# Optimization experiments

Measured on AMD Instinct MI355X. Metric: run time of the kernel, lower is better.

Reference implementation:

```python
import jax, jax.numpy as jnp
import numpy as np

N_NODES = 100000
N_EDGES = 1600000
D_IN = 128
D_HID = 128
SCALE = 1.8
EPS = 1e-12


def setup_inputs() -> dict:
    key = jax.random.key(0)
    ks = jax.random.split(key, 7)
    x = jax.random.normal(ks[0], (N_NODES, D_IN), dtype=jnp.float32)
    W1 = jax.random.normal(ks[1], (D_HID, D_IN), dtype=jnp.float32) * 0.05
    b1 = jax.random.normal(ks[2], (D_HID,), dtype=jnp.float32) * 0.05
    W2 = jax.random.normal(ks[3], (D_HID, D_HID), dtype=jnp.float32) * 0.05
    b2 = jax.random.normal(ks[4], (D_HID,), dtype=jnp.float32) * 0.05
    src = jax.random.randint(ks[5], (N_EDGES,), 0, N_NODES, dtype=jnp.int64 if jax.config.jax_enable_x64 else jnp.int32)
    dst = jax.random.randint(ks[6], (N_EDGES,), 0, N_NODES, dtype=jnp.int64 if jax.config.jax_enable_x64 else jnp.int32)
    return {"x": x, "W1": W1, "b1": b1, "W2": W2, "b2": b2, "src": src, "dst": dst}


def reference(x, W1, b1, W2, b2, src, dst):
    N = x.shape[0]
    ones = jnp.ones((src.shape[0],), dtype=x.dtype)
    # GraphConv norm='both' degree normalizers (clamped to >=1 as in DGL)
    deg_out = jnp.maximum(jnp.zeros((N,), x.dtype).at[src].add(ones), 1.0)
    deg_in = jnp.maximum(jnp.zeros((N,), x.dtype).at[dst].add(ones), 1.0)
    norm_out = jax.lax.rsqrt(deg_out)[:, None]  # [N,1]
    norm_in = jax.lax.rsqrt(deg_in)[:, None]    # [N,1]

    def layer(h, W, b):
        # torch.nn.Linear: h @ W.T + b
        h = jnp.einsum('nd,kd->nk', h, W) + b
        # F.normalize(h, dim=1) * 1.8
        nrm = jnp.sqrt(jnp.sum(h * h, axis=1, keepdims=True))
        h = h / jnp.maximum(nrm, EPS) * SCALE
        # GraphConv (weight=False, bias=False, norm='both'):
        # D_out^{-1/2} -> sparse aggregate -> D_in^{-1/2}
        h = h * norm_out
        agg = jax.ops.segment_sum(h[src], dst, num_segments=N)
        return agg * norm_in

    h = layer(x, W1, b1)
    h = layer(h, W2, b2)
    return h
```

## Files before the change

### kernel.cpp

```cpp
#include <hip/hip_runtime.h>
#include <cstdint>
#include <cstddef>

#define D 128
#define NSCALE 1.8f
#define NEPS 1e-12f
#define EPB 4096
#define NLO 512
#define SCAP 9216
#define SSTRIDE 10240
#define SRCB 23
#define SRCM 0x7FFFFF

typedef __attribute__((ext_vector_type(8))) short bf16x8;
typedef __attribute__((ext_vector_type(4))) float f32x4;

__device__ __forceinline__ ushort bf16_rtn(float f) {
    uint32_t u = __float_as_uint(f);
    u = u + 0x7FFFu + ((u >> 16) & 1u);
    return (ushort)(u >> 16);
}

__device__ __forceinline__ float blo(uint32_t u) { return __uint_as_float(u << 16); }
__device__ __forceinline__ float bhi(uint32_t u) { return __uint_as_float(u & 0xFFFF0000u); }

__global__ __launch_bounds__(512) void zero_kernel(int* __restrict__ p) {
    p[threadIdx.x] = 0;
}

__global__ __launch_bounds__(512) void scatter_direct_kernel(const int* __restrict__ src,
                                                             const int* __restrict__ dst,
                                                             int* __restrict__ cnt_d,
                                                             int* __restrict__ cnt_s,
                                                             uint32_t* __restrict__ spack,
                                                             ushort* __restrict__ ss_low,
                                                             int ne) {
    __shared__ int hist[256], sc[256], cur[256], gbase[256];
    __shared__ uint32_t sbuf[EPB];
    __shared__ uint8_t binb[EPB];
    int t = threadIdx.x, b = blockIdx.x;
    int base = b * EPB, end = min(ne, base + EPB), m = end - base;

    int myd[8], mys[8];
    #pragma unroll
    for (int k = 0; k < 8; ++k) {
        int i = base + t + 512 * k;
        bool ok = (i < end);
        myd[k] = ok ? dst[i] : -1;
        mys[k] = ok ? src[i] : -1;
    }

    if (t < 256) hist[t] = 0;
    __syncthreads();
    #pragma unroll
    for (int k = 0; k < 8; ++k)
        if (myd[k] >= 0) atomicAdd(&hist[myd[k] >> 9], 1);
    __syncthreads();
    if (t < 256) sc[t] = hist[t];
    __syncthreads();
    #pragma unroll
    for (int off = 1; off < 256; off <<= 1) {
        int u = (t >= off && t < 256) ? sc[t - off] : 0;
        __syncthreads();
        if (t < 256) sc[t] += u;
        __syncthreads();
    }
    if (t < 256) {
        int c = hist[t];
        int excl = sc[t] - c;
        cur[t] = excl;
        if (c > 0) {
            int ofs = atomicAdd(&cnt_d[t], c);
            gbase[t] = t * SSTRIDE + ofs - excl;
        }
    }
    __syncthreads();
    #pragma unroll
    for (int k = 0; k < 8; ++k) {
        if (myd[k] >= 0) {
            int bin = myd[k] >> 9;
            int pos = atomicAdd(&cur[bin], 1);
            sbuf[pos] = ((uint32_t)(myd[k] & (NLO - 1)) << SRCB) | (uint32_t)mys[k];
            binb[pos] = (uint8_t)bin;
        }
    }
    __syncthreads();
    for (int i = t; i < m; i += 512) {
        int bin = binb[i];
        int gi = gbase[bin] + i;
        if (gi - bin * SSTRIDE < SSTRIDE) spack[gi] = sbuf[i];
    }
    __syncthreads();

    if (t < 256) hist[t] = 0;
    __syncthreads();
    #pragma unroll
    for (int k = 0; k < 8; ++k)
        if (mys[k] >= 0) atomicAdd(&hist[mys[k] >> 9], 1);
    __syncthreads();
    if (t < 256) sc[t] = hist[t];
    __syncthreads();
    #pragma unroll
    for (int off = 1; off < 256; off <<= 1) {
        int u = (t >= off && t < 256) ? sc[t - off] : 0;
        __syncthreads();
        if (t < 256) sc[t] += u;
        __syncthreads();
    }
    if (t < 256) {
        int c = hist[t];
        int excl = sc[t] - c;
        cur[t] = excl;
        if (c > 0) {
            int ofs = atomicAdd(&cnt_s[t], c);
            gbase[t] = t * SSTRIDE + ofs - excl;
        }
    }
    __syncthreads();
    ushort* sb2 = (ushort*)sbuf;
    #pragma unroll
    for (int k = 0; k < 8; ++k) {
        if (mys[k] >= 0) {
            int bin = mys[k] >> 9;
            int pos = atomicAdd(&cur[bin], 1);
            sb2[pos] = (ushort)(mys[k] & (NLO - 1));
            binb[pos] = (uint8_t)bin;
        }
    }
    __syncthreads();
    for (int i = t; i < m; i += 512) {
        int bin = binb[i];
        int gi = gbase[bin] + i;
        if (gi - bin * SSTRIDE < SSTRIDE) ss_low[gi] = sb2[i];
    }
}

__global__ __launch_bounds__(1024) void bucket_sorthist_kernel(const uint32_t* __restrict__ spack,
                                                               const int* __restrict__ cnt_d,
                                                               const ushort* __restrict__ ss_low,
                                                               const int* __restrict__ cnt_s,
                                                               int* __restrict__ offs,
                                                               int* __restrict__ cnt_dst,
                                                               float* __restrict__ norm_in,
                                                               float* __restrict__ norm_out,
                                                               int* __restrict__ ssrc, int N) {
    __shared__ int h[NLO], sc[NLO], cur[NLO];
    __shared__ int inA[SCAP];
    __shared__ int stage[SCAP];
    int t = threadIdx.x, v = blockIdx.x;
    int beg = v * SSTRIDE;

    if (blockIdx.y == 1) {
        int m2 = min(cnt_s[v], SSTRIDE);
        int end = beg + m2;
        if (t < NLO) h[t] = 0;
        __syncthreads();
        for (int i = beg + t; i < end; i += 1024) atomicAdd(&h[(int)ss_low[i]], 1);
        __syncthreads();
        int g = (v << 9) + t;
        if (t < NLO && g < N) norm_out[g] = rsqrtf((float)max(h[t], 1));
        return;
    }

    int m = min(cnt_d[v], SSTRIDE);
    int end = beg + m;
    bool staged = (m <= SCAP);

    if (t < NLO) h[t] = 0;
    if (staged) {
        __syncthreads();
        for (int i = beg + t; i < end; i += 1024) inA[i - beg] = (int)spack[i];
        __syncthreads();
        for (int i = t; i < m; i += 1024) atomicAdd(&h[((uint32_t)inA[i]) >> SRCB], 1);
    } else {
        __syncthreads();
        for (int i = beg + t; i < end; i += 1024) atomicAdd(&h[spack[i] >> SRCB], 1);
    }
    __syncthreads();
    int cnt = 0;
    if (t < NLO) { cnt = h[t]; sc[t] = cnt; }
    __syncthreads();
    #pragma unroll
    for (int off = 1; off < NLO; off <<= 1) {
        int u = (t >= off && t < NLO) ? sc[t - off] : 0;
        __syncthreads();
        if (t < NLO) sc[t] += u;
        __syncthreads();
    }
    int excl = (t < NLO) ? (sc[t] - cnt) : 0;
    int g = (v << 9) + t;
    if (t < NLO && g < N) {
        offs[g] = beg + excl;
        cnt_dst[g] = cnt;
        norm_in[g] = rsqrtf((float)max(cnt, 1));
    }
    if (staged) {
        if (t < NLO) cur[t] = excl;
        __syncthreads();
        for (int i = t; i < m; i += 1024) {
            uint32_t p = (uint32_t)inA[i];
            int pos = atomicAdd(&cur[p >> SRCB], 1);
            stage[pos] = (int)(p & SRCM);
        }
        __syncthreads();
        for (int j = t; j < m; j += 1024) ssrc[beg + j] = stage[j];
    } else {
        if (t < NLO) cur[t] = beg + excl;
        __syncthreads();
        for (int i = beg + t; i < end; i += 1024) {
            uint32_t p = spack[i];
            int pos = atomicAdd(&cur[p >> SRCB], 1);
            ssrc[pos] = (int)(p & SRCM);
        }
    }
}

__global__ __launch_bounds__(256, 2) void mlp_fused_kernel(const float* __restrict__ X,
                                                           const float* __restrict__ W1,
                                                           const float* __restrict__ b1,
                                                           const float* __restrict__ W2,
                                                           const float* __restrict__ post,
                                                           ushort* __restrict__ Q,
                                                           ushort* __restrict__ Abuf, int N) {
    __shared__ ushort Wf1[128 * 128];
    __shared__ ushort Wf2[128 * 128];

    const int t = threadIdx.x;
    const int wave = t >> 6;
    const int lane = t & 63;
    const int q = lane >> 4;
    const int l16 = lane & 15;

    if (blockIdx.x == 0 && t < 32) {
        if (t < 16) ((uint4*)(Q    + (size_t)N * D))[t]      = make_uint4(0u, 0u, 0u, 0u);
        else        ((uint4*)(Abuf + (size_t)N * D))[t - 16] = make_uint4(0u, 0u, 0u, 0u);
    }

    #pragma unroll
    for (int it = 0; it < 8; ++it) {
        int f = t + 256 * it;
        int j = f >> 8;
        int p = (f >> 6) & 3;
        int ln = f & 63;
        int m = ln & 15;
        int k0 = 32 * p + 8 * (ln >> 4);
        {
            int row = 32 * (j >> 1) + 8 * (m >> 2) + 4 * (j & 1) + (m & 3);
            const float* srcp = W1 + row * D + k0;
            float4 a0 = *(const float4*)(srcp);
            float4 a1 = *(const float4*)(srcp + 4);
            bf16x8 v;
            v[0] = (short)bf16_rtn(a0.x); v[1] = (short)bf16_rtn(a0.y);
            v[2] = (short)bf16_rtn(a0.z); v[3] = (short)bf16_rtn(a0.w);
            v[4] = (short)bf16_rtn(a1.x); v[5] = (short)bf16_rtn(a1.y);
            v[6] = (short)bf16_rtn(a1.z); v[7] = (short)bf16_rtn(a1.w);
            ((bf16x8*)Wf1)[f] = v;
        }
        {
            int row = 16 * j + m;
            const float* srcp = W2 + row * D + k0;
            float4 a0 = *(const float4*)(srcp);
            float4 a1 = *(const float4*)(srcp + 4);
            bf16x8 v;
            v[0] = (short)bf16_rtn(a0.x); v[1] = (short)bf16_rtn(a0.y);
            v[2] = (short)bf16_rtn(a0.z); v[3] = (short)bf16_rtn(a0.w);
            v[4] = (short)bf16_rtn(a1.x); v[5] = (short)bf16_rtn(a1.y);
            v[6] = (short)bf16_rtn(a1.z); v[7] = (short)bf16_rtn(a1.w);
            ((bf16x8*)Wf2)[f] = v;
        }
    }

    const int r0 = blockIdx.x * 128 + wave * 32;
    bf16x8 xhi[2][4], xlo[2][4];
    #pragma unroll
    for (int rt = 0; rt < 2; ++rt) {
        int row = r0 + rt * 16 + l16;
        bool ok = (row < N);
        const float* xr = X + (size_t)(ok ? row : 0) * D;
        #pragma unroll
        for (int p = 0; p < 4; ++p) {
            int k0 = 32 * p + 8 * q;
            float4 a0 = ok ? *(const float4*)(xr + k0)     : make_float4(0, 0, 0, 0);
            float4 a1 = ok ? *(const float4*)(xr + k0 + 4) : make_float4(0, 0, 0, 0);
            float fv[8] = {a0.x, a0.y, a0.z, a0.w, a1.x, a1.y, a1.z, a1.w};
            bf16x8 h, l;
            #pragma unroll
            for (int e = 0; e < 8; ++e) {
                uint32_t u = __float_as_uint(fv[e]);
                h[e] = (short)(u >> 16);
                float hf = __uint_as_float(u & 0xFFFF0000u);
                l[e] = (short)(__float_as_uint(fv[e] - hf) >> 16);
            }
            xhi[rt][p] = h;
            xlo[rt][p] = l;
        }
    }

    __syncthreads();

    f32x4 acc1[2][8];
    #pragma unroll
    for (int rt = 0; rt < 2; ++rt)
        #pragma unroll
        for (int j = 0; j < 8; ++j) acc1[rt][j] = (f32x4){0.f, 0.f, 0.f, 0.f};

    #pragma unroll
    for (int p = 0; p < 4; ++p) {
        #pragma unroll
        for (int j = 0; j < 8; ++j) {
            bf16x8 wf = ((bf16x8*)Wf1)[(j * 4 + p) * 64 + lane];
            acc1[0][j] = __builtin_amdgcn_mfma_f32_16x16x32_bf16(wf, xhi[0][p], acc1[0][j], 0, 0, 0);
            acc1[0][j] = __builtin_amdgcn_mfma_f32_16x16x32_bf16(wf, xlo[0][p], acc1[0][j], 0, 0, 0);
            acc1[1][j] = __builtin_amdgcn_mfma_f32_16x16x32_bf16(wf, xhi[1][p], acc1[1][j], 0, 0, 0);
            acc1[1][j] = __builtin_amdgcn_mfma_f32_16x16x32_bf16(wf, xlo[1][p], acc1[1][j], 0, 0, 0);
        }
    }

    #pragma unroll
    for (int rt = 0; rt < 2; ++rt) {
        int node = r0 + rt * 16 + l16;
        float po = (node < N) ? post[node] : 0.f;
        float ss = 0.f;
        #pragma unroll
        for (int j = 0; j < 8; ++j) {
            const float4 bq = *(const float4*)(b1 + 32 * (j >> 1) + 8 * q + 4 * (j & 1));
            float v0 = acc1[rt][j][0] + bq.x; acc1[rt][j][0] = v0; ss += v0 * v0;
            float v1 = acc1[rt][j][1] + bq.y; acc1[rt][j][1] = v1; ss += v1 * v1;
            float v2 = acc1[rt][j][2] + bq.z; acc1[rt][j][2] = v2; ss += v2 * v2;
            float v3 = acc1[rt][j][3] + bq.w; acc1[rt][j][3] = v3; ss += v3 * v3;
        }
        ss += __shfl_xor(ss, 16);
        ss += __shfl_xor(ss, 32);
        float fsc = NSCALE / fmaxf(sqrtf(ss), NEPS) * po;
        #pragma unroll
        for (int j = 0; j < 8; ++j) {
            acc1[rt][j][0] *= fsc; acc1[rt][j][1] *= fsc;
            acc1[rt][j][2] *= fsc; acc1[rt][j][3] *= fsc;
        }
    }

    f32x4 acc2[2][8];
    #pragma unroll
    for (int rt = 0; rt < 2; ++rt)
        #pragma unroll
        for (int j = 0; j < 8; ++j) acc2[rt][j] = (f32x4){0.f, 0.f, 0.f, 0.f};

    #pragma unroll
    for (int p = 0; p < 4; ++p) {
        bf16x8 p2h0, p2l0, p2h1, p2l1;
        #pragma unroll
        for (int e = 0; e < 8; ++e) {
            float v0 = acc1[0][2 * p + (e >> 2)][e & 3];
            uint32_t u0 = __float_as_uint(v0);
            p2h0[e] = (short)(u0 >> 16);
            p2l0[e] = (short)(__float_as_uint(v0 - __uint_as_float(u0 & 0xFFFF0000u)) >> 16);
            float v1 = acc1[1][2 * p + (e >> 2)][e & 3];
            uint32_t u1 = __float_as_uint(v1);
            p2h1[e] = (short)(u1 >> 16);
            p2l1[e] = (short)(__float_as_uint(v1 - __uint_as_float(u1 & 0xFFFF0000u)) >> 16);
        }
        #pragma unroll
        for (int j = 0; j < 8; ++j) {
            bf16x8 wf = ((bf16x8*)Wf2)[(j * 4 + p) * 64 + lane];
            acc2[0][j] = __builtin_amdgcn_mfma_f32_16x16x32_bf16(wf, p2h0, acc2[0][j], 0, 0, 0);
            acc2[0][j] = __builtin_amdgcn_mfma_f32_16x16x32_bf16(wf, p2l0, acc2[0][j], 0, 0, 0);
            acc2[1][j] = __builtin_amdgcn_mfma_f32_16x16x32_bf16(wf, p2h1, acc2[1][j], 0, 0, 0);
            acc2[1][j] = __builtin_amdgcn_mfma_f32_16x16x32_bf16(wf, p2l1, acc2[1][j], 0, 0, 0);
        }
    }

    #pragma unroll
    for (int rt = 0; rt < 2; ++rt) {
        int node = r0 + rt * 16 + l16;
        if (node < N) {
            ushort* qp = Q + (size_t)node * D + 4 * q;
            #pragma unroll
            for (int j = 0; j < 8; ++j) {
                ushort4 s4;
                s4.x = bf16_rtn(acc2[rt][j][0]);
                s4.y = bf16_rtn(acc2[rt][j][1]);
                s4.z = bf16_rtn(acc2[rt][j][2]);
                s4.w = bf16_rtn(acc2[rt][j][3]);
                *(ushort4*)(qp + 16 * j) = s4;
            }
        }
    }
}

__global__ __launch_bounds__(256) void agg_mid_kernel(const ushort* __restrict__ A,
                                                      const int* __restrict__ sorted_src,
                                                      const int* __restrict__ offs,
                                                      const int* __restrict__ cnt,
                                                      const float* __restrict__ norm_in,
                                                      const float* __restrict__ norm_out,
                                                      const float* __restrict__ b2,
                                                      ushort* __restrict__ Abuf, int N) {
    int wave = threadIdx.x >> 6;
    int n0 = (blockIdx.x * 4 + wave) * 2;
    if (n0 >= N) return;
    int lane = threadIdx.x & 63;
    int g = lane >> 4;
    int c = lane & 15;
    const ushort* Ac = A + c * 8;

    int n1 = n0 + 1;
    int beg0 = offs[n0], len0 = cnt[n0];
    int beg1 = 0, len1 = 0;
    if (n1 < N) { beg1 = offs[n1]; len1 = cnt[n1]; }
    int last0 = beg0 + len0 - 1;
    int last1 = beg1 + len1 - 1;

    float a0[8] = {0.f, 0.f, 0.f, 0.f, 0.f, 0.f, 0.f, 0.f};
    float a1[8] = {0.f, 0.f, 0.f, 0.f, 0.f, 0.f, 0.f, 0.f};

    int mx = max(len0, len1);
    for (int i = 0; i < mx; i += 16) {
        int idx[8];
        #pragma unroll
        for (int k = 0; k < 4; ++k) {
            int e = beg0 + i + g + 4 * k;
            int cl = max(min(e, last0), 0);
            idx[k] = sorted_src[cl];
            if (e > last0) idx[k] = N;
        }
        #pragma unroll
        for (int k = 0; k < 4; ++k) {
            int e = beg1 + i + g + 4 * k;
            int cl = max(min(e, last1), 0);
            idx[4 + k] = sorted_src[cl];
            if (e > last1) idx[4 + k] = N;
        }
        uint4 w[8];
        #pragma unroll
        for (int k = 0; k < 8; ++k) w[k] = *(const uint4*)(Ac + (size_t)idx[k] * D);
        #pragma unroll
        for (int k = 0; k < 4; ++k) {
            a0[0] += blo(w[k].x); a0[1] += bhi(w[k].x);
            a0[2] += blo(w[k].y); a0[3] += bhi(w[k].y);
            a0[4] += blo(w[k].z); a0[5] += bhi(w[k].z);
            a0[6] += blo(w[k].w); a0[7] += bhi(w[k].w);
        }
        #pragma unroll
        for (int k = 4; k < 8; ++k) {
            a1[0] += blo(w[k].x); a1[1] += bhi(w[k].x);
            a1[2] += blo(w[k].y); a1[3] += bhi(w[k].y);
            a1[4] += blo(w[k].z); a1[5] += bhi(w[k].z);
            a1[6] += blo(w[k].w); a1[7] += bhi(w[k].w);
        }
    }

    #pragma unroll
    for (int e = 0; e < 8; ++e) {
        a0[e] += __shfl_xor(a0[e], 16);
        a0[e] += __shfl_xor(a0[e], 32);
        a1[e] += __shfl_xor(a1[e], 16);
        a1[e] += __shfl_xor(a1[e], 32);
    }

    float4 bql = *(const float4*)(b2 + c * 8);
    float4 bqh = *(const float4*)(b2 + c * 8 + 4);
    float bb[8] = {bql.x, bql.y, bql.z, bql.w, bqh.x, bqh.y, bqh.z, bqh.w};

    {
        float ni = norm_in[n0];
        float y[8];
        float ss = 0.f;
        #pragma unroll
        for (int e = 0; e < 8; ++e) { y[e] = a0[e] * ni + bb[e]; ss += y[e] * y[e]; }
        ss += __shfl_xor(ss, 1); ss += __shfl_xor(ss, 2);
        ss += __shfl_xor(ss, 4); ss += __shfl_xor(ss, 8);
        float fsc = NSCALE / fmaxf(sqrtf(ss), NEPS) * norm_out[n0];
        if (g == 0) {
            ushort4 s0, s1;
            s0.x = bf16_rtn(y[0] * fsc); s0.y = bf16_rtn(y[1] * fsc);
            s0.z = bf16_rtn(y[2] * fsc); s0.w = bf16_rtn(y[3] * fsc);
            s1.x = bf16_rtn(y[4] * fsc); s1.y = bf16_rtn(y[5] * fsc);
            s1.z = bf16_rtn(y[6] * fsc); s1.w = bf16_rtn(y[7] * fsc);
            ushort* op = Abuf + (size_t)n0 * D + c * 8;
            *(ushort4*)(op) = s0;
            *(ushort4*)(op + 4) = s1;
        }
    }
    if (n1 < N) {
        float ni = norm_in[n1];
        float y[8];
        float ss = 0.f;
        #pragma unroll
        for (int e = 0; e < 8; ++e) { y[e] = a1[e] * ni + bb[e]; ss += y[e] * y[e]; }
        ss += __shfl_xor(ss, 1); ss += __shfl_xor(ss, 2);
        ss += __shfl_xor(ss, 4); ss += __shfl_xor(ss, 8);
        float fsc = NSCALE / fmaxf(sqrtf(ss), NEPS) * norm_out[n1];
        if (g == 0) {
            ushort4 s0, s1;
            s0.x = bf16_rtn(y[0] * fsc); s0.y = bf16_rtn(y[1] * fsc);
            s0.z = bf16_rtn(y[2] * fsc); s0.w = bf16_rtn(y[3] * fsc);
            s1.x = bf16_rtn(y[4] * fsc); s1.y = bf16_rtn(y[5] * fsc);
            s1.z = bf16_rtn(y[6] * fsc); s1.w = bf16_rtn(y[7] * fsc);
            ushort* op = Abuf + (size_t)n1 * D + c * 8;
            *(ushort4*)(op) = s0;
            *(ushort4*)(op + 4) = s1;
        }
    }
}

__global__ __launch_bounds__(256) void agg_kernel(const ushort* __restrict__ A,
                                                  const int* __restrict__ sorted_src,
                                                  const int* __restrict__ offs,
                                                  const int* __restrict__ cnt,
                                                  const float* __restrict__ norm_in,
                                                  float* __restrict__ out, int N) {
    int wave = threadIdx.x >> 6;
    int n0 = (blockIdx.x * 4 + wave) * 2;
    if (n0 >= N) return;
    int lane = threadIdx.x & 63;
    int g = lane >> 4;
    int c = lane & 15;
    const ushort* Ac = A + c * 8;

    int n1 = n0 + 1;
    int beg0 = offs[n0], len0 = cnt[n0];
    int beg1 = 0, len1 = 0;
    if (n1 < N) { beg1 = offs[n1]; len1 = cnt[n1]; }
    int last0 = beg0 + len0 - 1;
    int last1 = beg1 + len1 - 1;

    float a0[8] = {0.f, 0.f, 0.f, 0.f, 0.f, 0.f, 0.f, 0.f};
    float a1[8] = {0.f, 0.f, 0.f, 0.f, 0.f, 0.f, 0.f, 0.f};

    int mx = max(len0, len1);
    for (int i = 0; i < mx; i += 16) {
        int idx[8];
        #pragma unroll
        for (int k = 0; k < 4; ++k) {
            int e = beg0 + i + g + 4 * k;
            int cl = max(min(e, last0), 0);
            idx[k] = sorted_src[cl];
            if (e > last0) idx[k] = N;
        }
        #pragma unroll
        for (int k = 0; k < 4; ++k) {
            int e = beg1 + i + g + 4 * k;
            int cl = max(min(e, last1), 0);
            idx[4 + k] = sorted_src[cl];
            if (e > last1) idx[4 + k] = N;
        }
        uint4 w[8];
        #pragma unroll
        for (int k = 0; k < 8; ++k) w[k] = *(const uint4*)(Ac + (size_t)idx[k] * D);
        #pragma unroll
        for (int k = 0; k < 4; ++k) {
            a0[0] += blo(w[k].x); a0[1] += bhi(w[k].x);
            a0[2] += blo(w[k].y); a0[3] += bhi(w[k].y);
            a0[4] += blo(w[k].z); a0[5] += bhi(w[k].z);
            a0[6] += blo(w[k].w); a0[7] += bhi(w[k].w);
        }
        #pragma unroll
        for (int k = 4; k < 8; ++k) {
            a1[0] += blo(w[k].x); a1[1] += bhi(w[k].x);
            a1[2] += blo(w[k].y); a1[3] += bhi(w[k].y);
            a1[4] += blo(w[k].z); a1[5] += bhi(w[k].z);
            a1[6] += blo(w[k].w); a1[7] += bhi(w[k].w);
        }
    }

    #pragma unroll
    for (int e = 0; e < 8; ++e) {
        a0[e] += __shfl_xor(a0[e], 16);
        a0[e] += __shfl_xor(a0[e], 32);
        a1[e] += __shfl_xor(a1[e], 16);
        a1[e] += __shfl_xor(a1[e], 32);
    }

    if (g == 0) {
        float sc0 = norm_in[n0];
        float* op0 = out + (size_t)n0 * D + c * 8;
        *(float4*)(op0)     = make_float4(a0[0] * sc0, a0[1] * sc0, a0[2] * sc0, a0[3] * sc0);
        *(float4*)(op0 + 4) = make_float4(a0[4] * sc0, a0[5] * sc0, a0[6] * sc0, a0[7] * sc0);
        if (n1 < N) {
            float sc1 = norm_in[n1];
            float* op1 = out + (size_t)n1 * D + c * 8;
            *(float4*)(op1)     = make_float4(a1[0] * sc1, a1[1] * sc1, a1[2] * sc1, a1[3] * sc1);
            *(float4*)(op1 + 4) = make_float4(a1[4] * sc1, a1[5] * sc1, a1[6] * sc1, a1[7] * sc1);
        }
    }
}


extern "C" void kernel_launch(void* const* d_in, const int* in_sizes, int n_in,
                              void* d_out, int out_size, void* d_ws, size_t ws_size,
                              hipStream_t stream) {
    const float* x  = (const float*)d_in[0];
    const float* W1 = (const float*)d_in[1];
    const float* b1 = (const float*)d_in[2];
    const float* W2 = (const float*)d_in[3];
    const float* b2 = (const float*)d_in[4];
    const int* src  = (const int*)d_in[5];
    const int* dst  = (const int*)d_in[6];
    float* out = (float*)d_out;

    const int N  = in_sizes[0] / D;
    const int NE = in_sizes[5];
    const int NBK = (NE + EPB - 1) / EPB;
    const int HB  = (N + NLO - 1) / NLO;

    char* w = (char*)d_ws;
    auto take = [&](size_t bytes) { char* p = w; w += (bytes + 255) & ~(size_t)255; return p; };
    int*      cnt2     = (int*)take(512 * 4);
    uint32_t* spack    = (uint32_t*)take((size_t)HB * SSTRIDE * 4);
    ushort*   ss_low   = (ushort*)take((size_t)HB * SSTRIDE * 2);
    int*      ssrc     = (int*)take((size_t)HB * SSTRIDE * 4);
    int*      offs     = (int*)take((size_t)N * 4);
    int*      cnt_dst  = (int*)take((size_t)N * 4);
    float*    norm_in  = (float*)take((size_t)N * 4);
    float*    norm_out = (float*)take((size_t)N * 4);
    ushort*   Qbuf     = (ushort*)take((size_t)(N + 1) * D * 2);
    ushort*   Abuf     = (ushort*)take((size_t)(N + 1) * D * 2);
    int* cnt_d = cnt2;
    int* cnt_s = cnt2 + 256;

    zero_kernel<<<1, 512, 0, stream>>>(cnt2);
    scatter_direct_kernel<<<NBK, 512, 0, stream>>>(src, dst, cnt_d, cnt_s,
                                                   spack, ss_low, NE);
    bucket_sorthist_kernel<<<dim3(HB, 2), 1024, 0, stream>>>(spack, cnt_d, ss_low, cnt_s,
                                                             offs, cnt_dst, norm_in,
                                                             norm_out, ssrc, N);

    const int mlp_blocks = (N + 127) / 128;
    const int agg_blocks = (N + 7) / 8;

    mlp_fused_kernel<<<mlp_blocks, 256, 0, stream>>>(x, W1, b1, W2, norm_out, Qbuf, Abuf, N);
    agg_mid_kernel<<<agg_blocks, 256, 0, stream>>>(Qbuf, ssrc, offs, cnt_dst,
                                                   norm_in, norm_out, b2, Abuf, N);
    agg_kernel<<<agg_blocks, 256, 0, stream>>>(Abuf, ssrc, offs, cnt_dst, norm_in, out, N);
}
```

Before: 290.8 us.

## Fuse edge scatter with first-layer MLP and apply norm_out during aggregation

Merges the edge bucket-scatter kernel and the MLP kernel into a single launch. Even blocks do the scatter and odd blocks run the MLP, sharing one LDS allocation, so the independent work overlaps on the GPU. To remove the MLP's dependence on norm_out, which is produced later, the out-degree scaling moves into agg_mid's gather loop. That loop now loads norm_out per neighbor and uses FMA, and a padded norm_out[N]=0 entry covers the sentinel index. The MLP blocks now handle 256 rows with 512 threads, which changes occupancy, and the gather loop pays for the extra per-edge scalar loads.

```diff
diff --git a/kernel.cpp b/kernel.cpp
--- a/kernel.cpp
+++ b/kernel.cpp
@@ -28,217 +28,148 @@
     p[threadIdx.x] = 0;
 }
 
-__global__ __launch_bounds__(512) void scatter_direct_kernel(const int* __restrict__ src,
+__global__ __launch_bounds__(512, 2) void scatter_mlp_kernel(const int* __restrict__ src,
                                                              const int* __restrict__ dst,
                                                              int* __restrict__ cnt_d,
                                                              int* __restrict__ cnt_s,
                                                              uint32_t* __restrict__ spack,
                                                              ushort* __restrict__ ss_low,
-                                                             int ne) {
-    __shared__ int hist[256], sc[256], cur[256], gbase[256];
-    __shared__ uint32_t sbuf[EPB];
-    __shared__ uint8_t binb[EPB];
-    int t = threadIdx.x, b = blockIdx.x;
-    int base = b * EPB, end = min(ne, base + EPB), m = end - base;
-
-    int myd[8], mys[8];
-    #pragma unroll
-    for (int k = 0; k < 8; ++k) {
-        int i = base + t + 512 * k;
-        bool ok = (i < end);
-        myd[k] = ok ? dst[i] : -1;
-        mys[k] = ok ? src[i] : -1;
-    }
-
-    if (t < 256) hist[t] = 0;
-    __syncthreads();
-    #pragma unroll
-    for (int k = 0; k < 8; ++k)
-        if (myd[k] >= 0) atomicAdd(&hist[myd[k] >> 9], 1);
-    __syncthreads();
-    if (t < 256) sc[t] = hist[t];
-    __syncthreads();
-    #pragma unroll
-    for (int off = 1; off < 256; off <<= 1) {
-        int u = (t >= off && t < 256) ? sc[t - off] : 0;
-        __syncthreads();
-        if (t < 256) sc[t] += u;
-        __syncthreads();
-    }
-    if (t < 256) {
-        int c = hist[t];
-        int excl = sc[t] - c;
-        cur[t] = excl;
-        if (c > 0) {
-            int ofs = atomicAdd(&cnt_d[t], c);
-            gbase[t] = t * SSTRIDE + ofs - excl;
-        }
-    }
-    __syncthreads();
-    #pragma unroll
-    for (int k = 0; k < 8; ++k) {
-        if (myd[k] >= 0) {
-            int bin = myd[k] >> 9;
-            int pos = atomicAdd(&cur[bin], 1);
-            sbuf[pos] = ((uint32_t)(myd[k] & (NLO - 1)) << SRCB) | (uint32_t)mys[k];
-            binb[pos] = (uint8_t)bin;
-        }
-    }
-    __syncthreads();
-    for (int i = t; i < m; i += 512) {
-        int bin = binb[i];
-        int gi = gbase[bin] + i;
-        if (gi - bin * SSTRIDE < SSTRIDE) spack[gi] = sbuf[i];
-    }
-    __syncthreads();
-
-    if (t < 256) hist[t] = 0;
-    __syncthreads();
-    #pragma unroll
-    for (int k = 0; k < 8; ++k)
-        if (mys[k] >= 0) atomicAdd(&hist[mys[k] >> 9], 1);
-    __syncthreads();
-    if (t < 256) sc[t] = hist[t];
-    __syncthreads();
-    #pragma unroll
-    for (int off = 1; off < 256; off <<= 1) {
-        int u = (t >= off && t < 256) ? sc[t - off] : 0;
-        __syncthreads();
-        if (t < 256) sc[t] += u;
-        __syncthreads();
-    }
-    if (t < 256) {
-        int c = hist[t];
-        int excl = sc[t] - c;
-        cur[t] = excl;
-        if (c > 0) {
-            int ofs = atomicAdd(&cnt_s[t], c);
-            gbase[t] = t * SSTRIDE + ofs - excl;
-        }
-    }
-    __syncthreads();
-    ushort* sb2 = (ushort*)sbuf;
-    #pragma unroll
-    for (int k = 0; k < 8; ++k) {
-        if (mys[k] >= 0) {
-            int bin = mys[k] >> 9;
-            int pos = atomicAdd(&cur[bin], 1);
-            sb2[pos] = (ushort)(mys[k] & (NLO - 1));
-            binb[pos] = (uint8_t)bin;
-        }
-    }
-    __syncthreads();
-    for (int i = t; i < m; i += 512) {
-        int bin = binb[i];
-        int gi = gbase[bin] + i;
-        if (gi - bin * SSTRIDE < SSTRIDE) ss_low[gi] = sb2[i];
-    }
-}
-
-__global__ __launch_bounds__(1024) void bucket_sorthist_kernel(const uint32_t* __restrict__ spack,
-                                                               const int* __restrict__ cnt_d,
-                                                               const ushort* __restrict__ ss_low,
-                                                               const int* __restrict__ cnt_s,
-                                                               int* __restrict__ offs,
-                                                               int* __restrict__ cnt_dst,
-                                                               float* __restrict__ norm_in,
-                                                               float* __restrict__ norm_out,
-                                                               int* __restrict__ ssrc, int N) {
-    __shared__ int h[NLO], sc[NLO], cur[NLO];
-    __shared__ int inA[SCAP];
-    __shared__ int stage[SCAP];
-    int t = threadIdx.x, v = blockIdx.x;
-    int beg = v * SSTRIDE;
-
-    if (blockIdx.y == 1) {
-        int m2 = min(cnt_s[v], SSTRIDE);
-        int end = beg + m2;
-        if (t < NLO) h[t] = 0;
-        __syncthreads();
-        for (int i = beg + t; i < end; i += 1024) atomicAdd(&h[(int)ss_low[i]], 1);
-        __syncthreads();
-        int g = (v << 9) + t;
-        if (t < NLO && g < N) norm_out[g] = rsqrtf((float)max(h[t], 1));
+                                                             int ne,
+                                                             const float* __restrict__ X,
+                                                             const float* __restrict__ W1,
+                                                             const float* __restrict__ b1,
+                                                             const float* __restrict__ W2,
+                                                             ushort* __restrict__ Q,
+                                                             ushort* __restrict__ Abuf,
+                                                             int N, int sb, int mb) {
+    __shared__ ushort Wf[2][128 * 128];
+
+    const int t = threadIdx.x;
+    const int bid = blockIdx.x;
+
+    if ((bid & 1) == 0) {
+        int b = bid >> 1;
+        if (b >= sb) return;
+        char* ldsc = (char*)Wf;
+        int* hist  = (int*)ldsc;
+        int* sc    = (int*)(ldsc + 1024);
+        int* cur   = (int*)(ldsc + 2048);
+        int* gbase = (int*)(ldsc + 3072);
+        uint32_t* sbuf = (uint32_t*)(ldsc + 4096);
+        uint8_t*  binb = (uint8_t*)(ldsc + 4096 + EPB * 4);
+
+        int base = b * EPB, end = min(ne, base + EPB), m = end - base;
+
+        int myd[8], mys[8];
+        #pragma unroll
+        for (int k = 0; k < 8; ++k) {
+            int i = base + t + 512 * k;
+            bool ok = (i < end);
+            myd[k] = ok ? dst[i] : -1;
+            mys[k] = ok ? src[i] : -1;
+        }
+
+        if (t < 256) hist[t] = 0;
+        __syncthreads();
+        #pragma unroll
+        for (int k = 0; k < 8; ++k)
+            if (myd[k] >= 0) atomicAdd(&hist[myd[k] >> 9], 1);
+        __syncthreads();
+        if (t < 256) sc[t] = hist[t];
+        __syncthreads();
+        #pragma unroll
+        for (int off = 1; off < 256; off <<= 1) {
+            int u = (t >= off && t < 256) ? sc[t - off] : 0;
+            __syncthreads();
+            if (t < 256) sc[t] += u;
+            __syncthreads();
+        }
+        if (t < 256) {
+            int c = hist[t];
+            int excl = sc[t] - c;
+            cur[t] = excl;
+            if (c > 0) {
+                int ofs = atomicAdd(&cnt_d[t], c);
+                gbase[t] = t * SSTRIDE + ofs - excl;
+            }
+        }
+        __syncthreads();
+        #pragma unroll
+        for (int k = 0; k < 8; ++k) {
+            if (myd[k] >= 0) {
+                int bin = myd[k] >> 9;
+                int pos = atomicAdd(&cur[bin], 1);
+                sbuf[pos] = ((uint32_t)(myd[k] & (NLO - 1)) << SRCB) | (uint32_t)mys[k];
+                binb[pos] = (uint8_t)bin;
+            }
+        }
+        __syncthreads();
+        for (int i = t; i < m; i += 512) {
+            int bin = binb[i];
+            int gi = gbase[bin] + i;
+            if (gi - bin * SSTRIDE < SSTRIDE) spack[gi] = sbuf[i];
+        }
+        __syncthreads();
+
+        if (t < 256) hist[t] = 0;
+        __syncthreads();
+        #pragma unroll
+        for (int k = 0; k < 8; ++k)
+            if (mys[k] >= 0) atomicAdd(&hist[mys[k] >> 9], 1);
+        __syncthreads();
+        if (t < 256) sc[t] = hist[t];
+        __syncthreads();
+        #pragma unroll
+        for (int off = 1; off < 256; off <<= 1) {
+            int u = (t >= off && t < 256) ? sc[t - off] : 0;
+            __syncthreads();
+            if (t < 256) sc[t] += u;
+            __syncthreads();
+        }
+        if (t < 256) {
+            int c = hist[t];
+            int excl = sc[t] - c;
+            cur[t] = excl;
+            if (c > 0) {
+                int ofs = atomicAdd(&cnt_s[t], c);
+                gbase[t] = t * SSTRIDE + ofs - excl;
+            }
+        }
+        __syncthreads();
+        ushort* sb2 = (ushort*)sbuf;
+        #pragma unroll
+        for (int k = 0; k < 8; ++k) {
+            if (mys[k] >= 0) {
+                int bin = mys[k] >> 9;
+                int pos = atomicAdd(&cur[bin], 1);
+                sb2[pos] = (ushort)(mys[k] & (NLO - 1));
+                binb[pos] = (uint8_t)bin;
+            }
+        }
+        __syncthreads();
+        for (int i = t; i < m; i += 512) {
+            int bin = binb[i];
+            int gi = gbase[bin] + i;
+            if (gi - bin * SSTRIDE < SSTRIDE) ss_low[gi] = sb2[i];
+        }
         return;
     }
 
-    int m = min(cnt_d[v], SSTRIDE);
-    int end = beg + m;
-    bool staged = (m <= SCAP);
-
-    if (t < NLO) h[t] = 0;
-    if (staged) {
-        __syncthreads();
-        for (int i = beg + t; i < end; i += 1024) inA[i - beg] = (int)spack[i];
-        __syncthreads();
-        for (int i = t; i < m; i += 1024) atomicAdd(&h[((uint32_t)inA[i]) >> SRCB], 1);
-    } else {
-        __syncthreads();
-        for (int i = beg + t; i < end; i += 1024) atomicAdd(&h[spack[i] >> SRCB], 1);
-    }
-    __syncthreads();
-    int cnt = 0;
-    if (t < NLO) { cnt = h[t]; sc[t] = cnt; }
-    __syncthreads();
-    #pragma unroll
-    for (int off = 1; off < NLO; off <<= 1) {
-        int u = (t >= off && t < NLO) ? sc[t - off] : 0;
-        __syncthreads();
-        if (t < NLO) sc[t] += u;
-        __syncthreads();
-    }
-    int excl = (t < NLO) ? (sc[t] - cnt) : 0;
-    int g = (v << 9) + t;
-    if (t < NLO && g < N) {
-        offs[g] = beg + excl;
-        cnt_dst[g] = cnt;
-        norm_in[g] = rsqrtf((float)max(cnt, 1));
-    }
-    if (staged) {
-        if (t < NLO) cur[t] = excl;
-        __syncthreads();
-        for (int i = t; i < m; i += 1024) {
-            uint32_t p = (uint32_t)inA[i];
-            int pos = atomicAdd(&cur[p >> SRCB], 1);
-            stage[pos] = (int)(p & SRCM);
-        }
-        __syncthreads();
-        for (int j = t; j < m; j += 1024) ssrc[beg + j] = stage[j];
-    } else {
-        if (t < NLO) cur[t] = beg + excl;
-        __syncthreads();
-        for (int i = beg + t; i < end; i += 1024) {
-            uint32_t p = spack[i];
-            int pos = atomicAdd(&cur[p >> SRCB], 1);
-            ssrc[pos] = (int)(p & SRCM);
-        }
-    }
-}
-
-__global__ __launch_bounds__(256, 2) void mlp_fused_kernel(const float* __restrict__ X,
-                                                           const float* __restrict__ W1,
-                                                           const float* __restrict__ b1,
-                                                           const float* __restrict__ W2,
-                                                           const float* __restrict__ post,
-                                                           ushort* __restrict__ Q,
-                                                           ushort* __restrict__ Abuf, int N) {
-    __shared__ ushort Wf1[128 * 128];
-    __shared__ ushort Wf2[128 * 128];
-
-    const int t = threadIdx.x;
+    int mbid = bid >> 1;
+    if (mbid >= mb) return;
     const int wave = t >> 6;
     const int lane = t & 63;
     const int q = lane >> 4;
     const int l16 = lane & 15;
 
-    if (blockIdx.x == 0 && t < 32) {
+    if (mbid == 0 && t < 32) {
         if (t < 16) ((uint4*)(Q    + (size_t)N * D))[t]      = make_uint4(0u, 0u, 0u, 0u);
         else        ((uint4*)(Abuf + (size_t)N * D))[t - 16] = make_uint4(0u, 0u, 0u, 0u);
     }
 
     #pragma unroll
-    for (int it = 0; it < 8; ++it) {
-        int f = t + 256 * it;
+    for (int it = 0; it < 4; ++it) {
+        int f = t + 512 * it;
         int j = f >> 8;
         int p = (f >> 6) & 3;
         int ln = f & 63;
@@ -254,7 +185,7 @@
             v[2] = (short)bf16_rtn(a0.z); v[3] = (short)bf16_rtn(a0.w);
             v[4] = (short)bf16_rtn(a1.x); v[5] = (short)bf16_rtn(a1.y);
             v[6] = (short)bf16_rtn(a1.z); v[7] = (short)bf16_rtn(a1.w);
-            ((bf16x8*)Wf1)[f] = v;
+            ((bf16x8*)Wf[0])[f] = v;
         }
         {
             int row = 16 * j + m;
@@ -266,11 +197,11 @@
             v[2] = (short)bf16_rtn(a0.z); v[3] = (short)bf16_rtn(a0.w);
             v[4] = (short)bf16_rtn(a1.x); v[5] = (short)bf16_rtn(a1.y);
             v[6] = (short)bf16_rtn(a1.z); v[7] = (short)bf16_rtn(a1.w);
-            ((bf16x8*)Wf2)[f] = v;
-        }
-    }
-
-    const int r0 = blockIdx.x * 128 + wave * 32;
+            ((bf16x8*)Wf[1])[f] = v;
+        }
+    }
+
+    const int r0 = mbid * 256 + wave * 32;
     bf16x8 xhi[2][4], xlo[2][4];
     #pragma unroll
     for (int rt = 0; rt < 2; ++rt) {
@@ -308,7 +239,7 @@
     for (int p = 0; p < 4; ++p) {
         #pragma unroll
         for (int j = 0; j < 8; ++j) {
-            bf16x8 wf = ((bf16x8*)Wf1)[(j * 4 + p) * 64 + lane];
+            bf16x8 wf = ((bf16x8*)Wf[0])[(j * 4 + p) * 64 + lane];
             acc1[0][j] = __builtin_amdgcn_mfma_f32_16x16x32_bf16(wf, xhi[0][p], acc1[0][j], 0, 0, 0);
             acc1[0][j] = __builtin_amdgcn_mfma_f32_16x16x32_bf16(wf, xlo[0][p], acc1[0][j], 0, 0, 0);
             acc1[1][j] = __builtin_amdgcn_mfma_f32_16x16x32_bf16(wf, xhi[1][p], acc1[1][j], 0, 0, 0);
@@ -318,8 +249,6 @@
 
     #pragma unroll
     for (int rt = 0; rt < 2; ++rt) {
-        int node = r0 + rt * 16 + l16;
-        float po = (node < N) ? post[node] : 0.f;
         float ss = 0.f;
         #pragma unroll
         for (int j = 0; j < 8; ++j) {
@@ -331,7 +260,7 @@
         }
         ss += __shfl_xor(ss, 16);
         ss += __shfl_xor(ss, 32);
-        float fsc = NSCALE / fmaxf(sqrtf(ss), NEPS) * po;
+        float fsc = NSCALE / fmaxf(sqrtf(ss), NEPS);
         #pragma unroll
         for (int j = 0; j < 8; ++j) {
             acc1[rt][j][0] *= fsc; acc1[rt][j][1] *= fsc;
@@ -361,7 +290,7 @@
         }
         #pragma unroll
         for (int j = 0; j < 8; ++j) {
-            bf16x8 wf = ((bf16x8*)Wf2)[(j * 4 + p) * 64 + lane];
+            bf16x8 wf = ((bf16x8*)Wf[1])[(j * 4 + p) * 64 + lane];
             acc2[0][j] = __builtin_amdgcn_mfma_f32_16x16x32_bf16(wf, p2h0, acc2[0][j], 0, 0, 0);
             acc2[0][j] = __builtin_amdgcn_mfma_f32_16x16x32_bf16(wf, p2l0, acc2[0][j], 0, 0, 0);
             acc2[1][j] = __builtin_amdgcn_mfma_f32_16x16x32_bf16(wf, p2h1, acc2[1][j], 0, 0, 0);
@@ -383,6 +312,87 @@
                 s4.w = bf16_rtn(acc2[rt][j][3]);
                 *(ushort4*)(qp + 16 * j) = s4;
             }
+        }
+    }
+}
+
+__global__ __launch_bounds__(1024) void bucket_sorthist_kernel(const uint32_t* __restrict__ spack,
+                                                               const int* __restrict__ cnt_d,
+                                                               const ushort* __restrict__ ss_low,
+                                                               const int* __restrict__ cnt_s,
+                                                               int* __restrict__ offs,
+                                                               int* __restrict__ cnt_dst,
+                                                               float* __restrict__ norm_in,
+                                                               float* __restrict__ norm_out,
+                                                               int* __restrict__ ssrc, int N) {
+    __shared__ int h[NLO], sc[NLO], cur[NLO];
+    __shared__ int inA[SCAP];
+    __shared__ int stage[SCAP];
+    int t = threadIdx.x, v = blockIdx.x;
+    int beg = v * SSTRIDE;
+
+    if (blockIdx.y == 1) {
+        if (v == 0 && t == 0) norm_out[N] = 0.f;
+        int m2 = min(cnt_s[v], SSTRIDE);
+        int end = beg + m2;
+        if (t < NLO) h[t] = 0;
+        __syncthreads();
+        for (int i = beg + t; i < end; i += 1024) atomicAdd(&h[(int)ss_low[i]], 1);
+        __syncthreads();
+        int g = (v << 9) + t;
+        if (t < NLO && g < N) norm_out[g] = rsqrtf((float)max(h[t], 1));
+        return;
+    }
+
+    int m = min(cnt_d[v], SSTRIDE);
+    int end = beg + m;
+    bool staged = (m <= SCAP);
+
+    if (t < NLO) h[t] = 0;
+    if (staged) {
+        __syncthreads();
+        for (int i = beg + t; i < end; i += 1024) inA[i - beg] = (int)spack[i];
+        __syncthreads();
+        for (int i = t; i < m; i += 1024) atomicAdd(&h[((uint32_t)inA[i]) >> SRCB], 1);
+    } else {
+        __syncthreads();
+        for (int i = beg + t; i < end; i += 1024) atomicAdd(&h[spack[i] >> SRCB], 1);
+    }
+    __syncthreads();
+    int cnt = 0;
+    if (t < NLO) { cnt = h[t]; sc[t] = cnt; }
+    __syncthreads();
+    #pragma unroll
+    for (int off = 1; off < NLO; off <<= 1) {
+        int u = (t >= off && t < NLO) ? sc[t - off] : 0;
+        __syncthreads();
+        if (t < NLO) sc[t] += u;
+        __syncthreads();
+    }
+    int excl = (t < NLO) ? (sc[t] - cnt) : 0;
+    int g = (v << 9) + t;
+    if (t < NLO && g < N) {
+        offs[g] = beg + excl;
+        cnt_dst[g] = cnt;
+        norm_in[g] = rsqrtf((float)max(cnt, 1));
+    }
+    if (staged) {
+        if (t < NLO) cur[t] = excl;
+        __syncthreads();
+        for (int i = t; i < m; i += 1024) {
+            uint32_t p = (uint32_t)inA[i];
+            int pos = atomicAdd(&cur[p >> SRCB], 1);
+            stage[pos] = (int)(p & SRCM);
+        }
+        __syncthreads();
+        for (int j = t; j < m; j += 1024) ssrc[beg + j] = stage[j];
+    } else {
+        if (t < NLO) cur[t] = beg + excl;
+        __syncthreads();
+        for (int i = beg + t; i < end; i += 1024) {
+            uint32_t p = spack[i];
+            int pos = atomicAdd(&cur[p >> SRCB], 1);
+            ssrc[pos] = (int)(p & SRCM);
         }
     }
 }
@@ -431,21 +441,25 @@
             if (e > last1) idx[4 + k] = N;
         }
         uint4 w[8];
-        #pragma unroll
-        for (int k = 0; k < 8; ++k) w[k] = *(const uint4*)(Ac + (size_t)idx[k] * D);
+        float sn[8];
+        #pragma unroll
+        for (int k = 0; k < 8; ++k) {
+            w[k] = *(const uint4*)(Ac + (size_t)idx[k] * D);
+            sn[k] = norm_out[idx[k]];
+        }
         #pragma unroll
         for (int k = 0; k < 4; ++k) {
-            a0[0] += blo(w[k].x); a0[1] += bhi(w[k].x);
-            a0[2] += blo(w[k].y); a0[3] += bhi(w[k].y);
-            a0[4] += blo(w[k].z); a0[5] += bhi(w[k].z);
-            a0[6] += blo(w[k].w); a0[7] += bhi(w[k].w);
+            a0[0] = fmaf(blo(w[k].x), sn[k], a0[0]); a0[1] = fmaf(bhi(w[k].x), sn[k], a0[1]);
+            a0[2] = fmaf(blo(w[k].y), sn[k], a0[2]); a0[3] = fmaf(bhi(w[k].y), sn[k], a0[3]);
+            a0[4] = fmaf(blo(w[k].z), sn[k], a0[4]); a0[5] = fmaf(bhi(w[k].z), sn[k], a0[5]);
+            a0[6] = fmaf(blo(w[k].w), sn[k], a0[6]); a0[7] = fmaf(bhi(w[k].w), sn[k], a0[7]);
         }
         #pragma unroll
         for (int k = 4; k < 8; ++k) {
-            a1[0] += blo(w[k].x); a1[1] += bhi(w[k].x);
-            a1[2] += blo(w[k].y); a1[3] += bhi(w[k].y);
-            a1[4] += blo(w[k].z); a1[5] += bhi(w[k].z);
-            a1[6] += blo(w[k].w); a1[7] += bhi(w[k].w);
+            a1[0] = fmaf(blo(w[k].x), sn[k], a1[0]); a1[1] = fmaf(bhi(w[k].x), sn[k], a1[1]);
+            a1[2] = fmaf(blo(w[k].y), sn[k], a1[2]); a1[3] = fmaf(bhi(w[k].y), sn[k], a1[3]);
+            a1[4] = fmaf(blo(w[k].z), sn[k], a1[4]); a1[5] = fmaf(bhi(w[k].z), sn[k], a1[5]);
+            a1[6] = fmaf(blo(w[k].w), sn[k], a1[6]); a1[7] = fmaf(bhi(w[k].w), sn[k], a1[7]);
         }
     }
 
@@ -600,7 +614,8 @@
 
     const int N  = in_sizes[0] / D;
     const int NE = in_sizes[5];
-    const int NBK = (NE + EPB - 1) / EPB;
+    const int SB  = (NE + EPB - 1) / EPB;
+    const int MB  = (N + 255) / 256;
     const int HB  = (N + NLO - 1) / NLO;
 
     char* w = (char*)d_ws;
@@ -612,23 +627,23 @@
     int*      offs     = (int*)take((size_t)N * 4);
     int*      cnt_dst  = (int*)take((size_t)N * 4);
     float*    norm_in  = (float*)take((size_t)N * 4);
-    float*    norm_out = (float*)take((size_t)N * 4);
+    float*    norm_out = (float*)take((size_t)(N + 1) * 4);
     ushort*   Qbuf     = (ushort*)take((size_t)(N + 1) * D * 2);
     ushort*   Abuf     = (ushort*)take((size_t)(N + 1) * D * 2);
     int* cnt_d = cnt2;
     int* cnt_s = cnt2 + 256;
 
+    const int fb = 2 * max(SB, MB);
+
     zero_kernel<<<1, 512, 0, stream>>>(cnt2);
-    scatter_direct_kernel<<<NBK, 512, 0, stream>>>(src, dst, cnt_d, cnt_s,
-                                                   spack, ss_low, NE);
+    scatter_mlp_kernel<<<fb, 512, 0, stream>>>(src, dst, cnt_d, cnt_s, spack, ss_low, NE,
+                                               x, W1, b1, W2, Qbuf, Abuf, N, SB, MB);
     bucket_sorthist_kernel<<<dim3(HB, 2), 1024, 0, stream>>>(spack, cnt_d, ss_low, cnt_s,
                                                              offs, cnt_dst, norm_in,
                                                              norm_out, ssrc, N);
 
-    const int mlp_blocks = (N + 127) / 128;
     const int agg_blocks = (N + 7) / 8;
 
-    mlp_fused_kernel<<<mlp_blocks, 256, 0, stream>>>(x, W1, b1, W2, norm_out, Qbuf, Abuf, N);
     agg_mid_kernel<<<agg_blocks, 256, 0, stream>>>(Qbuf, ssrc, offs, cnt_dst,
                                                    norm_in, norm_out, b2, Abuf, N);
     agg_kernel<<<agg_blocks, 256, 0, stream>>>(Abuf, ssrc, offs, cnt_dst, norm_in, out, N);
```

After: 295.4 us. Within noise of the previous version (+1.6%).
